# Optimization experiments

Hardware: AMD Instinct MI355X
Metric: run time of the kernel (lower is better)

## Reference

```python
import jax, jax.numpy as jnp
import numpy as np

B, S, D = 8, 4096, 256


def setup_inputs() -> dict:
    key = jax.random.key(0)
    kq, kk, kv, kb = jax.random.split(key, 4)
    q = jax.random.normal(kq, (B, S, D), dtype=jnp.float32)
    k = jax.random.normal(kk, (B, S, D), dtype=jnp.float32)
    v = jax.random.normal(kv, (B, S, D), dtype=jnp.float32)
    beta = jax.random.uniform(kb, (B, S), dtype=jnp.float32)
    return {"q": q, "k": k, "v": v, "beta": beta}


def reference(q, k, v, beta):
    # Delta-rule linear attention recurrence:
    #   h_t = beta_t * h_{t-1} + k_t^T v_t   (h: [B, D, D])
    #   o_t = q_t @ h_t                      (o: [B, D])
    dtype = q.dtype
    b, s, d = q.shape
    h0 = jnp.zeros((b, d, d), dtype=dtype)

    def step(h, inp):
        q_t, k_t, v_t, b_t = inp  # q_t/k_t/v_t: [B, D], b_t: [B]
        h = h * b_t[:, None, None] + jnp.einsum('bi,bj->bij', k_t, v_t)
        o_t = jnp.einsum('bi,bij->bj', q_t, h)
        return h, o_t

    xs = (q.transpose(1, 0, 2), k.transpose(1, 0, 2),
          v.transpose(1, 0, 2), beta.T)  # time-major
    _, out = jax.lax.scan(step, h0, xs)  # out: [S, B, D]
    return out.transpose(1, 0, 2)  # [B, S, D]
```

## Files before the change

### kernel.cpp

```cpp
#include <hip/hip_runtime.h>
#include <hip/hip_bf16.h>
#include <math.h>


#define B_ 8
#define S_ 4096
#define D_ 256
#define L_ 128
#define C_ (S_ / L_)
#define BC_ (B_ * C_)
#define STK 66

typedef __attribute__((ext_vector_type(8))) short s8v;
typedef __attribute__((ext_vector_type(4))) float f4v;
typedef unsigned short u16;
typedef unsigned int u32;

__device__ __forceinline__ u32 pk2(float lo, float hi) {
  union { __hip_bfloat162 h; u32 u; } cv;
  cv.h = __float22bfloat162_rn(make_float2(lo, hi));
  return cv.u;
}
__device__ __forceinline__ s8v pack8(const float4 a, const float4 b) {
  union { u32 u[4]; s8v v; } r;
  r.u[0] = pk2(a.x, a.y); r.u[1] = pk2(a.z, a.w);
  r.u[2] = pk2(b.x, b.y); r.u[3] = pk2(b.z, b.w);
  return r.v;
}

__device__ __forceinline__ void beta_scan128(const float* betap, float* ls,
                                             int tid) {
  if (tid < 64) {
    float x = log2f(fmaxf(betap[tid], 1e-30f));
#pragma unroll
    for (int off = 1; off < 64; off <<= 1) {
      float y = __shfl_up(x, off);
      if (tid >= off) x += y;
    }
    ls[tid] = x;
    const float tot0 = __shfl(x, 63);
    float z = log2f(fmaxf(betap[64 + tid], 1e-30f));
#pragma unroll
    for (int off = 1; off < 64; off <<= 1) {
      float y = __shfl_up(z, off);
      if (tid >= off) z += y;
    }
    ls[64 + tid] = z + tot0;
  }
}

__global__ __launch_bounds__(512, 2) void ks_summary6(
    const float* __restrict__ kg, const float* __restrict__ vg,
    const float* __restrict__ beta, u16* __restrict__ A,
    float* __restrict__ P)
{
  __shared__ float ls[L_];
  __shared__ __align__(16) u16 U[2][256 * STK];
  __shared__ __align__(16) u16 BN[64 * 264];

  const int bc = blockIdx.x;
  const int b = bc / C_, c = bc % C_;
  const int tid = threadIdx.x;
  const float* betap = beta + (size_t)b * S_ + (size_t)c * L_;
  const float* kbase = kg + ((size_t)b * S_ + (size_t)c * L_) * D_;
  const float* vbase = vg + ((size_t)b * S_ + (size_t)c * L_) * D_;

  beta_scan128(betap, ls, tid);
  __syncthreads();
  const float ltot = ls[L_ - 1];
  if (tid == 0) P[bc] = exp2f(ltot);

  const int hh = tid >> 8;
  const int t2 = tid & 255;
  const int iLs = t2 & 7;
  const int s0s = (t2 >> 3) * 2;
  const int sg = hh * 64 + s0s;

  {
    const float* src0 = kbase + (size_t)sg * D_;
    const float* src1 = src0 + D_;
    const float w0 = exp2f(ltot - ls[sg]);
    const float w1 = exp2f(ltot - ls[sg + 1]);
    u16* dst = U[hh];
#pragma unroll
    for (int p = 0; p < 8; ++p) {
      const int i0 = p * 32 + iLs * 4;
      float a0[4], a1[4];
      *(float4*)a0 = *(const float4*)(src0 + i0);
      *(float4*)a1 = *(const float4*)(src1 + i0);
#pragma unroll
      for (int u = 0; u < 4; ++u)
        *(u32*)&dst[(i0 + u) * STK + s0s] = pk2(a0[u] * w0, a1[u] * w1);
    }
  }
  __syncthreads();

  const int lane = tid & 63, wave = tid >> 6;
  const int quad = lane >> 4, l15 = lane & 15;
  const int i0w = wave * 32;

  s8v af[2][4];
#pragma unroll
  for (int mt = 0; mt < 2; ++mt)
#pragma unroll
    for (int ks = 0; ks < 4; ++ks)
      af[mt][ks] = *(const s8v*)&U[ks >> 1][(i0w + mt * 16 + l15) * STK +
                                            (ks & 1) * 32 + quad * 8];
  __syncthreads();

  {
    const float* src0 = vbase + (size_t)sg * D_;
    const float* src1 = src0 + D_;
    u16* dst = U[hh];
#pragma unroll
    for (int p = 0; p < 8; ++p) {
      const int i0 = p * 32 + iLs * 4;
      float a0[4], a1[4];
      *(float4*)a0 = *(const float4*)(src0 + i0);
      *(float4*)a1 = *(const float4*)(src1 + i0);
#pragma unroll
      for (int u = 0; u < 4; ++u)
        *(u32*)&dst[(i0 + u) * STK + s0s] = pk2(a0[u], a1[u]);
    }
  }
  __syncthreads();

  u16* Ab = A + (size_t)bc * D_ * D_;

  for (int ng = 0; ng < 4; ++ng) {
    f4v acc[2][4];
#pragma unroll
    for (int mt = 0; mt < 2; ++mt)
#pragma unroll
      for (int nt = 0; nt < 4; ++nt) acc[mt][nt] = (f4v){0.f, 0.f, 0.f, 0.f};

#pragma unroll
    for (int ks = 0; ks < 4; ++ks) {
      const int so = (ks & 1) * 32 + quad * 8;
      s8v bv[4];
#pragma unroll
      for (int nt = 0; nt < 4; ++nt)
        bv[nt] = *(const s8v*)&U[ks >> 1][(ng * 64 + nt * 16 + l15) * STK + so];
#pragma unroll
      for (int mt = 0; mt < 2; ++mt)
#pragma unroll
        for (int nt = 0; nt < 4; ++nt)
          acc[mt][nt] = __builtin_amdgcn_mfma_f32_16x16x32_bf16(
              af[mt][ks], bv[nt], acc[mt][nt], 0, 0, 0);
    }
#pragma unroll
    for (int mt = 0; mt < 2; ++mt)
#pragma unroll
      for (int nt = 0; nt < 4; ++nt) {
        const int jl = nt * 16 + l15;
        uint2 w;
        w.x = pk2(acc[mt][nt][0], acc[mt][nt][1]);
        w.y = pk2(acc[mt][nt][2], acc[mt][nt][3]);
        *(uint2*)&BN[jl * 264 + i0w + mt * 16 + quad * 4] = w;
      }
    __syncthreads();
    {
      const int jl = tid >> 3;
      const int il = (tid & 7) * 8;
#pragma unroll
      for (int p = 0; p < 4; ++p) {
        const int iu = il + p * 64;
        *(s8v*)&Ab[(size_t)(ng * 64 + jl) * D_ + iu] =
            *(const s8v*)&BN[jl * 264 + iu];
      }
    }
    __syncthreads();
  }
}

__global__ __launch_bounds__(256) void ks_scan6(
    u16* __restrict__ A, const float* __restrict__ P)
{
  const int g = blockIdx.x;
  const int b = g >> 6;
  const int unit = ((g & 63) << 8) + threadIdx.x;
  u16* base = A + (size_t)b * ((size_t)C_ * D_ * D_) + (size_t)unit * 4;
  const float* Pb = P + b * C_;

  uint2 d[C_];
#pragma unroll
  for (int c = 0; c < C_; ++c)
    d[c] = *(const uint2*)(base + (size_t)c * (D_ * D_));

  float h0 = 0.f, h1 = 0.f, h2 = 0.f, h3 = 0.f;
#pragma unroll
  for (int c = 0; c < C_; ++c) {
    const float pc = Pb[c];
    const uint2 u = d[c];
    const float a0 = __uint_as_float(u.x << 16);
    const float a1 = __uint_as_float(u.x & 0xFFFF0000u);
    const float a2 = __uint_as_float(u.y << 16);
    const float a3 = __uint_as_float(u.y & 0xFFFF0000u);
    d[c].x = pk2(h0, h1);
    d[c].y = pk2(h2, h3);
    h0 = fmaf(pc, h0, a0); h1 = fmaf(pc, h1, a1);
    h2 = fmaf(pc, h2, a2); h3 = fmaf(pc, h3, a3);
  }
#pragma unroll
  for (int c = 0; c < C_; ++c)
    *(uint2*)(base + (size_t)c * (D_ * D_)) = d[c];
}

__global__ __launch_bounds__(512, 2) void ks_output6(
    const float* __restrict__ qg, const float* __restrict__ kg,
    const float* __restrict__ vg, const float* __restrict__ beta,
    const u16* __restrict__ Hg, float* __restrict__ outg)
{
  __shared__ float ls[L_];
  __shared__ float cv[L_];
  __shared__ __align__(16) u16 QB[L_ * 264];
  __shared__ __align__(16) u16 Tm[L_ * 136];
  __shared__ __align__(16) u16 VT[256 * STK];

  const int bc = blockIdx.x;
  const int b = bc / C_, c = bc % C_;
  const int tid = threadIdx.x;
  const float* betap = beta + (size_t)b * S_ + (size_t)c * L_;
  const float* qbase = qg + ((size_t)b * S_ + (size_t)c * L_) * D_;
  const float* kbase = kg + ((size_t)b * S_ + (size_t)c * L_) * D_;
  const float* vbase = vg + ((size_t)b * S_ + (size_t)c * L_) * D_;
  const u16* Hb = Hg + (size_t)bc * D_ * D_;

  beta_scan128(betap, ls, tid);

  {
    const int t = tid >> 2;
    const int cg = (tid & 3) * 8;
    const float* src = qbase + (size_t)t * D_ + cg;
#pragma unroll
    for (int p = 0; p < 8; ++p) {
      const s8v pk = pack8(*(const float4*)(src + p * 32),
                           *(const float4*)(src + p * 32 + 4));
      *(s8v*)&QB[t * 264 + cg + p * 32] = pk;
    }
  }
  __syncthreads();
  if (tid < L_) cv[tid] = exp2f(ls[tid]);

  const int lane = tid & 63, wave = tid >> 6;
  const int quad = lane >> 4, l15 = lane & 15;
  const int j0w = wave * 32;

  {
    const int mA = wave * 16;
    f4v accA[8];
#pragma unroll
    for (int i = 0; i < 8; ++i) accA[i] = (f4v){0.f, 0.f, 0.f, 0.f};
#pragma unroll
    for (int kd = 0; kd < 8; ++kd) {
      const int d0 = kd * 32 + quad * 8;
      const float* krow = kbase + (size_t)(mA + l15) * D_ + d0;
      const s8v af = pack8(*(const float4*)krow, *(const float4*)(krow + 4));
#pragma unroll
      for (int nt = 0; nt < 8; ++nt) {
        const s8v bf = *(const s8v*)&QB[(nt * 16 + l15) * 264 + d0];
        accA[nt] = __builtin_amdgcn_mfma_f32_16x16x32_bf16(af, bf, accA[nt],
                                                           0, 0, 0);
      }
    }
#pragma unroll
    for (int nt = 0; nt < 8; ++nt) {
      const int t = nt * 16 + l15;
      const float lt = ls[t];
      const int s0 = mA + quad * 4;
      float v[4];
#pragma unroll
      for (int r = 0; r < 4; ++r) {
        const int s = s0 + r;
        v[r] = (s <= t) ? accA[nt][r] * exp2f(lt - ls[s]) : 0.f;
      }
      uint2 w;
      w.x = pk2(v[0], v[1]);
      w.y = pk2(v[2], v[3]);
      *(uint2*)&Tm[t * 136 + s0] = w;
    }
  }

  {
    const int iL = tid & 15;
    const int s0 = ((tid >> 4) & 31) * 2;
    const float* src0 = vbase + (size_t)s0 * D_;
    const float* src1 = src0 + D_;
#pragma unroll
    for (int p = 0; p < 4; ++p) {
      const int i0 = p * 64 + iL * 4;
      float a0[4], a1[4];
      *(float4*)a0 = *(const float4*)(src0 + i0);
      *(float4*)a1 = *(const float4*)(src1 + i0);
#pragma unroll
      for (int u = 0; u < 4; ++u)
        *(u32*)&VT[(i0 + u) * STK + s0] = pk2(a0[u], a1[u]);
    }
  }

  s8v hc[2];
#pragma unroll
  for (int mt = 0; mt < 2; ++mt)
    hc[mt] = *(const s8v*)(Hb + (size_t)(j0w + mt * 16 + l15) * D_ + quad * 8);

  __syncthreads();

  f4v acc[2][8];
#pragma unroll
  for (int mt = 0; mt < 2; ++mt)
#pragma unroll
    for (int nt = 0; nt < 8; ++nt) acc[mt][nt] = (f4v){0.f, 0.f, 0.f, 0.f};

#pragma unroll
  for (int ks = 0; ks < 8; ++ks) {
    const int io = ks * 32 + quad * 8;
    s8v hn[2] = {hc[0], hc[1]};
    if (ks < 7) {
#pragma unroll
      for (int mt = 0; mt < 2; ++mt)
        hn[mt] = *(const s8v*)(Hb + (size_t)(j0w + mt * 16 + l15) * D_ +
                               io + 32);
    }
    s8v bf[8];
#pragma unroll
    for (int nt = 0; nt < 8; ++nt)
      bf[nt] = *(const s8v*)&QB[(nt * 16 + l15) * 264 + io];
#pragma unroll
    for (int mt = 0; mt < 2; ++mt)
#pragma unroll
      for (int nt = 0; nt < 8; ++nt)
        acc[mt][nt] = __builtin_amdgcn_mfma_f32_16x16x32_bf16(
            hc[mt], bf[nt], acc[mt][nt], 0, 0, 0);
    hc[0] = hn[0]; hc[1] = hn[1];
  }
#pragma unroll
  for (int nt = 0; nt < 8; ++nt) {
    const float ct = cv[nt * 16 + l15];
#pragma unroll
    for (int mt = 0; mt < 2; ++mt) {
      acc[mt][nt][0] *= ct; acc[mt][nt][1] *= ct;
      acc[mt][nt][2] *= ct; acc[mt][nt][3] *= ct;
    }
  }

#pragma unroll
  for (int ks = 0; ks < 2; ++ks) {
    const int so = ks * 32 + quad * 8;
    s8v af[2], bf[8];
#pragma unroll
    for (int mt = 0; mt < 2; ++mt)
      af[mt] = *(const s8v*)&VT[(j0w + mt * 16 + l15) * STK + so];
#pragma unroll
    for (int nt = 0; nt < 8; ++nt)
      bf[nt] = *(const s8v*)&Tm[(nt * 16 + l15) * 136 + so];
#pragma unroll
    for (int mt = 0; mt < 2; ++mt)
#pragma unroll
      for (int nt = 0; nt < 8; ++nt)
        acc[mt][nt] = __builtin_amdgcn_mfma_f32_16x16x32_bf16(
            af[mt], bf[nt], acc[mt][nt], 0, 0, 0);
  }

  __syncthreads();
  {
    const int iL = tid & 15;
    const int s0 = ((tid >> 4) & 31) * 2;
    const float* src0 = vbase + (size_t)(64 + s0) * D_;
    const float* src1 = src0 + D_;
#pragma unroll
    for (int p = 0; p < 4; ++p) {
      const int i0 = p * 64 + iL * 4;
      float a0[4], a1[4];
      *(float4*)a0 = *(const float4*)(src0 + i0);
      *(float4*)a1 = *(const float4*)(src1 + i0);
#pragma unroll
      for (int u = 0; u < 4; ++u)
        *(u32*)&VT[(i0 + u) * STK + s0] = pk2(a0[u], a1[u]);
    }
  }
  __syncthreads();
#pragma unroll
  for (int ks = 0; ks < 2; ++ks) {
    const int so = ks * 32 + quad * 8;
    s8v af[2], bf[8];
#pragma unroll
    for (int mt = 0; mt < 2; ++mt)
      af[mt] = *(const s8v*)&VT[(j0w + mt * 16 + l15) * STK + so];
#pragma unroll
    for (int nt = 0; nt < 8; ++nt)
      bf[nt] = *(const s8v*)&Tm[(nt * 16 + l15) * 136 + 64 + so];
#pragma unroll
    for (int mt = 0; mt < 2; ++mt)
#pragma unroll
      for (int nt = 0; nt < 8; ++nt)
        acc[mt][nt] = __builtin_amdgcn_mfma_f32_16x16x32_bf16(
            af[mt], bf[nt], acc[mt][nt], 0, 0, 0);
  }

  float* ob = outg + ((size_t)b * S_ + (size_t)c * L_) * D_;
#pragma unroll
  for (int mt = 0; mt < 2; ++mt)
#pragma unroll
    for (int nt = 0; nt < 8; ++nt) {
      const int t = nt * 16 + l15;
      const int j0 = j0w + mt * 16 + quad * 4;
      float4 o;
      o.x = acc[mt][nt][0]; o.y = acc[mt][nt][1];
      o.z = acc[mt][nt][2]; o.w = acc[mt][nt][3];
      *(float4*)(ob + (size_t)t * D_ + j0) = o;
    }
}

extern "C" void kernel_launch(void* const* d_in, const int* in_sizes, int n_in,
                              void* d_out, int out_size, void* d_ws,
                              size_t ws_size, hipStream_t stream) {
  const float* q = (const float*)d_in[0];
  const float* k = (const float*)d_in[1];
  const float* v = (const float*)d_in[2];
  const float* beta = (const float*)d_in[3];
  float* out = (float*)d_out;

  u16* A = (u16*)d_ws;
  float* P = (float*)((char*)d_ws + (size_t)BC_ * D_ * D_ * sizeof(u16));

  ks_summary6<<<dim3(BC_), dim3(512), 0, stream>>>(k, v, beta, A, P);
  ks_scan6<<<dim3(512), dim3(256), 0, stream>>>(A, P);
  ks_output6<<<dim3(BC_), dim3(512), 0, stream>>>(q, k, v, beta, A, out);
}
```

Baseline: 172.0 us.

## Split summary and output kernels across two blocks per chunk for more parallelism

Both the chunk-summary and output kernels now launch two blocks per chunk: the summary kernel splits the output j columns in half, and the output kernel splits the 128 timesteps into two halves of 64. Shared memory per block is reduced (a single staging buffer, smaller QB/Tm/VT tiles with V staged in 32-row slices), and launch bounds are raised to allow 4 blocks per CU. With only 256 blocks before, the intent is to fill the GPU's CUs better and raise occupancy. In exchange, the K chunk (summary) and the beta scan plus intra-chunk K·Q work (output) are duplicated across the paired blocks, and the output kernel adds extra barriers.

Result: slower. 192.0 us (+11.6%).

```diff
diff --git a/kernel.cpp b/kernel.cpp
--- a/kernel.cpp
+++ b/kernel.cpp
@@ -9,7 +9,6 @@
 #define L_ 128
 #define C_ (S_ / L_)
 #define BC_ (B_ * C_)
-#define STK 66
 
 typedef __attribute__((ext_vector_type(8))) short s8v;
 typedef __attribute__((ext_vector_type(4))) float f4v;
@@ -49,16 +48,17 @@
   }
 }
 
-__global__ __launch_bounds__(512, 2) void ks_summary6(
+__global__ __launch_bounds__(512, 4) void ks_summary7(
     const float* __restrict__ kg, const float* __restrict__ vg,
     const float* __restrict__ beta, u16* __restrict__ A,
     float* __restrict__ P)
 {
   __shared__ float ls[L_];
-  __shared__ __align__(16) u16 U[2][256 * STK];
+  __shared__ __align__(16) u16 SB[256 * 66];
   __shared__ __align__(16) u16 BN[64 * 264];
 
-  const int bc = blockIdx.x;
+  const int bx = blockIdx.x;
+  const int bc = bx >> 1, jh = bx & 1;
   const int b = bc / C_, c = bc % C_;
   const int tid = threadIdx.x;
   const float* betap = beta + (size_t)b * S_ + (size_t)c * L_;
@@ -68,66 +68,71 @@
   beta_scan128(betap, ls, tid);
   __syncthreads();
   const float ltot = ls[L_ - 1];
-  if (tid == 0) P[bc] = exp2f(ltot);
-
-  const int hh = tid >> 8;
-  const int t2 = tid & 255;
-  const int iLs = t2 & 7;
-  const int s0s = (t2 >> 3) * 2;
-  const int sg = hh * 64 + s0s;
-
-  {
-    const float* src0 = kbase + (size_t)sg * D_;
-    const float* src1 = src0 + D_;
-    const float w0 = exp2f(ltot - ls[sg]);
-    const float w1 = exp2f(ltot - ls[sg + 1]);
-    u16* dst = U[hh];
-#pragma unroll
-    for (int p = 0; p < 8; ++p) {
-      const int i0 = p * 32 + iLs * 4;
-      float a0[4], a1[4];
-      *(float4*)a0 = *(const float4*)(src0 + i0);
-      *(float4*)a1 = *(const float4*)(src1 + i0);
-#pragma unroll
-      for (int u = 0; u < 4; ++u)
-        *(u32*)&dst[(i0 + u) * STK + s0s] = pk2(a0[u] * w0, a1[u] * w1);
-    }
-  }
-  __syncthreads();
+  if (tid == 0 && jh == 0) P[bc] = exp2f(ltot);
 
   const int lane = tid & 63, wave = tid >> 6;
   const int quad = lane >> 4, l15 = lane & 15;
   const int i0w = wave * 32;
 
   s8v af[2][4];
-#pragma unroll
-  for (int mt = 0; mt < 2; ++mt)
-#pragma unroll
-    for (int ks = 0; ks < 4; ++ks)
-      af[mt][ks] = *(const s8v*)&U[ks >> 1][(i0w + mt * 16 + l15) * STK +
-                                            (ks & 1) * 32 + quad * 8];
+
+#pragma unroll
+  for (int h = 0; h < 2; ++h) {
+    {
+      const int iL = tid & 15;
+      const int s0 = (tid >> 4) * 2;
+      const int sg = h * 64 + s0;
+      const float* src0 = kbase + (size_t)sg * D_;
+      const float* src1 = src0 + D_;
+      const float w0 = exp2f(ltot - ls[sg]);
+      const float w1 = exp2f(ltot - ls[sg + 1]);
+#pragma unroll
+      for (int p = 0; p < 4; ++p) {
+        const int i0 = p * 64 + iL * 4;
+        float a0[4], a1[4];
+        *(float4*)a0 = *(const float4*)(src0 + i0);
+        *(float4*)a1 = *(const float4*)(src1 + i0);
+#pragma unroll
+        for (int u = 0; u < 4; ++u)
+          *(u32*)&SB[(i0 + u) * 66 + s0] = pk2(a0[u] * w0, a1[u] * w1);
+      }
+    }
+    __syncthreads();
+#pragma unroll
+    for (int mt = 0; mt < 2; ++mt)
+#pragma unroll
+      for (int kk = 0; kk < 2; ++kk)
+        af[mt][h * 2 + kk] = *(const s8v*)&SB[(i0w + mt * 16 + l15) * 66 +
+                                              kk * 32 + quad * 8];
+    __syncthreads();
+  }
+
+  {
+    const int jL = tid & 15;
+    const int sp = tid >> 4;
+#pragma unroll
+    for (int h = 0; h < 2; ++h) {
+      const int s0 = sp * 2;
+      const int sg = h * 64 + s0;
+      const float* src0 = vbase + (size_t)sg * D_ + jh * 128;
+      const float* src1 = src0 + D_;
+#pragma unroll
+      for (int p = 0; p < 2; ++p) {
+        const int j0 = p * 64 + jL * 4;
+        float a0[4], a1[4];
+        *(float4*)a0 = *(const float4*)(src0 + j0);
+        *(float4*)a1 = *(const float4*)(src1 + j0);
+#pragma unroll
+        for (int u = 0; u < 4; ++u)
+          *(u32*)&SB[h * (128 * 66) + (j0 + u) * 66 + s0] = pk2(a0[u], a1[u]);
+      }
+    }
+  }
   __syncthreads();
 
-  {
-    const float* src0 = vbase + (size_t)sg * D_;
-    const float* src1 = src0 + D_;
-    u16* dst = U[hh];
-#pragma unroll
-    for (int p = 0; p < 8; ++p) {
-      const int i0 = p * 32 + iLs * 4;
-      float a0[4], a1[4];
-      *(float4*)a0 = *(const float4*)(src0 + i0);
-      *(float4*)a1 = *(const float4*)(src1 + i0);
-#pragma unroll
-      for (int u = 0; u < 4; ++u)
-        *(u32*)&dst[(i0 + u) * STK + s0s] = pk2(a0[u], a1[u]);
-    }
-  }
-  __syncthreads();
-
   u16* Ab = A + (size_t)bc * D_ * D_;
 
-  for (int ng = 0; ng < 4; ++ng) {
+  for (int ng = 0; ng < 2; ++ng) {
     f4v acc[2][4];
 #pragma unroll
     for (int mt = 0; mt < 2; ++mt)
@@ -140,7 +145,8 @@
       s8v bv[4];
 #pragma unroll
       for (int nt = 0; nt < 4; ++nt)
-        bv[nt] = *(const s8v*)&U[ks >> 1][(ng * 64 + nt * 16 + l15) * STK + so];
+        bv[nt] = *(const s8v*)&SB[(ks >> 1) * (128 * 66) +
+                                  (ng * 64 + nt * 16 + l15) * 66 + so];
 #pragma unroll
       for (int mt = 0; mt < 2; ++mt)
 #pragma unroll
@@ -162,18 +168,18 @@
     {
       const int jl = tid >> 3;
       const int il = (tid & 7) * 8;
+      const int jgl = jh * 128 + ng * 64 + jl;
 #pragma unroll
       for (int p = 0; p < 4; ++p) {
         const int iu = il + p * 64;
-        *(s8v*)&Ab[(size_t)(ng * 64 + jl) * D_ + iu] =
-            *(const s8v*)&BN[jl * 264 + iu];
-      }
-    }
-    __syncthreads();
-  }
-}
-
-__global__ __launch_bounds__(256) void ks_scan6(
+        *(s8v*)&Ab[(size_t)jgl * D_ + iu] = *(const s8v*)&BN[jl * 264 + iu];
+      }
+    }
+    __syncthreads();
+  }
+}
+
+__global__ __launch_bounds__(256) void ks_scan7(
     u16* __restrict__ A, const float* __restrict__ P)
 {
   const int g = blockIdx.x;
@@ -206,18 +212,19 @@
     *(uint2*)(base + (size_t)c * (D_ * D_)) = d[c];
 }
 
-__global__ __launch_bounds__(512, 2) void ks_output6(
+__global__ __launch_bounds__(512, 4) void ks_output7(
     const float* __restrict__ qg, const float* __restrict__ kg,
     const float* __restrict__ vg, const float* __restrict__ beta,
     const u16* __restrict__ Hg, float* __restrict__ outg)
 {
   __shared__ float ls[L_];
-  __shared__ float cv[L_];
-  __shared__ __align__(16) u16 QB[L_ * 264];
-  __shared__ __align__(16) u16 Tm[L_ * 136];
-  __shared__ __align__(16) u16 VT[256 * STK];
-
-  const int bc = blockIdx.x;
+  __shared__ float cv[64];
+  __shared__ __align__(16) u16 QB[64 * 264];
+  __shared__ __align__(16) u16 Tm[64 * 136];
+  __shared__ __align__(16) u16 VT[256 * 34];
+
+  const int bx = blockIdx.x;
+  const int bc = bx >> 1, th = bx & 1;
   const int b = bc / C_, c = bc % C_;
   const int tid = threadIdx.x;
   const float* betap = beta + (size_t)b * S_ + (size_t)c * L_;
@@ -229,87 +236,34 @@
   beta_scan128(betap, ls, tid);
 
   {
-    const int t = tid >> 2;
-    const int cg = (tid & 3) * 8;
-    const float* src = qbase + (size_t)t * D_ + cg;
-#pragma unroll
-    for (int p = 0; p < 8; ++p) {
-      const s8v pk = pack8(*(const float4*)(src + p * 32),
-                           *(const float4*)(src + p * 32 + 4));
-      *(s8v*)&QB[t * 264 + cg + p * 32] = pk;
+    const int t_loc = tid >> 3;
+    const int d8 = (tid & 7) * 8;
+    const float* src = qbase + (size_t)(th * 64 + t_loc) * D_;
+#pragma unroll
+    for (int p = 0; p < 4; ++p) {
+      const int d0 = d8 + p * 64;
+      const s8v pk = pack8(*(const float4*)(src + d0),
+                           *(const float4*)(src + d0 + 4));
+      *(s8v*)&QB[t_loc * 264 + d0] = pk;
     }
   }
   __syncthreads();
-  if (tid < L_) cv[tid] = exp2f(ls[tid]);
+  if (tid < 64) cv[tid] = exp2f(ls[th * 64 + tid]);
 
   const int lane = tid & 63, wave = tid >> 6;
   const int quad = lane >> 4, l15 = lane & 15;
   const int j0w = wave * 32;
 
-  {
-    const int mA = wave * 16;
-    f4v accA[8];
-#pragma unroll
-    for (int i = 0; i < 8; ++i) accA[i] = (f4v){0.f, 0.f, 0.f, 0.f};
-#pragma unroll
-    for (int kd = 0; kd < 8; ++kd) {
-      const int d0 = kd * 32 + quad * 8;
-      const float* krow = kbase + (size_t)(mA + l15) * D_ + d0;
-      const s8v af = pack8(*(const float4*)krow, *(const float4*)(krow + 4));
-#pragma unroll
-      for (int nt = 0; nt < 8; ++nt) {
-        const s8v bf = *(const s8v*)&QB[(nt * 16 + l15) * 264 + d0];
-        accA[nt] = __builtin_amdgcn_mfma_f32_16x16x32_bf16(af, bf, accA[nt],
-                                                           0, 0, 0);
-      }
-    }
-#pragma unroll
-    for (int nt = 0; nt < 8; ++nt) {
-      const int t = nt * 16 + l15;
-      const float lt = ls[t];
-      const int s0 = mA + quad * 4;
-      float v[4];
-#pragma unroll
-      for (int r = 0; r < 4; ++r) {
-        const int s = s0 + r;
-        v[r] = (s <= t) ? accA[nt][r] * exp2f(lt - ls[s]) : 0.f;
-      }
-      uint2 w;
-      w.x = pk2(v[0], v[1]);
-      w.y = pk2(v[2], v[3]);
-      *(uint2*)&Tm[t * 136 + s0] = w;
-    }
-  }
-
-  {
-    const int iL = tid & 15;
-    const int s0 = ((tid >> 4) & 31) * 2;
-    const float* src0 = vbase + (size_t)s0 * D_;
-    const float* src1 = src0 + D_;
-#pragma unroll
-    for (int p = 0; p < 4; ++p) {
-      const int i0 = p * 64 + iL * 4;
-      float a0[4], a1[4];
-      *(float4*)a0 = *(const float4*)(src0 + i0);
-      *(float4*)a1 = *(const float4*)(src1 + i0);
-#pragma unroll
-      for (int u = 0; u < 4; ++u)
-        *(u32*)&VT[(i0 + u) * STK + s0] = pk2(a0[u], a1[u]);
-    }
-  }
+  f4v acc[2][4];
+#pragma unroll
+  for (int mt = 0; mt < 2; ++mt)
+#pragma unroll
+    for (int nt = 0; nt < 4; ++nt) acc[mt][nt] = (f4v){0.f, 0.f, 0.f, 0.f};
 
   s8v hc[2];
 #pragma unroll
   for (int mt = 0; mt < 2; ++mt)
     hc[mt] = *(const s8v*)(Hb + (size_t)(j0w + mt * 16 + l15) * D_ + quad * 8);
-
-  __syncthreads();
-
-  f4v acc[2][8];
-#pragma unroll
-  for (int mt = 0; mt < 2; ++mt)
-#pragma unroll
-    for (int nt = 0; nt < 8; ++nt) acc[mt][nt] = (f4v){0.f, 0.f, 0.f, 0.f};
 
 #pragma unroll
   for (int ks = 0; ks < 8; ++ks) {
@@ -321,20 +275,20 @@
         hn[mt] = *(const s8v*)(Hb + (size_t)(j0w + mt * 16 + l15) * D_ +
                                io + 32);
     }
-    s8v bf[8];
-#pragma unroll
-    for (int nt = 0; nt < 8; ++nt)
+    s8v bf[4];
+#pragma unroll
+    for (int nt = 0; nt < 4; ++nt)
       bf[nt] = *(const s8v*)&QB[(nt * 16 + l15) * 264 + io];
 #pragma unroll
     for (int mt = 0; mt < 2; ++mt)
 #pragma unroll
-      for (int nt = 0; nt < 8; ++nt)
+      for (int nt = 0; nt < 4; ++nt)
         acc[mt][nt] = __builtin_amdgcn_mfma_f32_16x16x32_bf16(
             hc[mt], bf[nt], acc[mt][nt], 0, 0, 0);
     hc[0] = hn[0]; hc[1] = hn[1];
   }
 #pragma unroll
-  for (int nt = 0; nt < 8; ++nt) {
+  for (int nt = 0; nt < 4; ++nt) {
     const float ct = cv[nt * 16 + l15];
 #pragma unroll
     for (int mt = 0; mt < 2; ++mt) {
@@ -343,71 +297,92 @@
     }
   }
 
-#pragma unroll
-  for (int ks = 0; ks < 2; ++ks) {
-    const int so = ks * 32 + quad * 8;
-    s8v af[2], bf[8];
-#pragma unroll
-    for (int mt = 0; mt < 2; ++mt)
-      af[mt] = *(const s8v*)&VT[(j0w + mt * 16 + l15) * STK + so];
-#pragma unroll
-    for (int nt = 0; nt < 8; ++nt)
-      bf[nt] = *(const s8v*)&Tm[(nt * 16 + l15) * 136 + so];
-#pragma unroll
-    for (int mt = 0; mt < 2; ++mt)
-#pragma unroll
-      for (int nt = 0; nt < 8; ++nt)
+  {
+    const int mA = wave * 16;
+    f4v accA[4];
+#pragma unroll
+    for (int i = 0; i < 4; ++i) accA[i] = (f4v){0.f, 0.f, 0.f, 0.f};
+#pragma unroll
+    for (int kd = 0; kd < 8; ++kd) {
+      const int d0 = kd * 32 + quad * 8;
+      const float* krow = kbase + (size_t)(mA + l15) * D_ + d0;
+      const s8v afr = pack8(*(const float4*)krow, *(const float4*)(krow + 4));
+#pragma unroll
+      for (int nt = 0; nt < 4; ++nt) {
+        const s8v bf = *(const s8v*)&QB[(nt * 16 + l15) * 264 + d0];
+        accA[nt] = __builtin_amdgcn_mfma_f32_16x16x32_bf16(afr, bf, accA[nt],
+                                                           0, 0, 0);
+      }
+    }
+#pragma unroll
+    for (int nt = 0; nt < 4; ++nt) {
+      const int t_loc = nt * 16 + l15;
+      const int t = th * 64 + t_loc;
+      const float lt = ls[t];
+      const int s0 = mA + quad * 4;
+      float v[4];
+#pragma unroll
+      for (int r = 0; r < 4; ++r) {
+        const int s = s0 + r;
+        v[r] = (s <= t) ? accA[nt][r] * exp2f(lt - ls[s]) : 0.f;
+      }
+      uint2 w;
+      w.x = pk2(v[0], v[1]);
+      w.y = pk2(v[2], v[3]);
+      *(uint2*)&Tm[t_loc * 136 + s0] = w;
+    }
+  }
+
+#pragma unroll
+  for (int sq = 0; sq < 4; ++sq) {
+    __syncthreads();
+    {
+      const int jL = tid & 15;
+      const int sp = (tid >> 4) & 15;
+      const int hb = tid >> 8;
+      const int s0 = sp * 2;
+      const int sg = sq * 32 + s0;
+      const float* src0 = vbase + (size_t)sg * D_;
+      const float* src1 = src0 + D_;
+#pragma unroll
+      for (int p = 0; p < 2; ++p) {
+        const int j0 = hb * 128 + p * 64 + jL * 4;
+        float a0[4], a1[4];
+        *(float4*)a0 = *(const float4*)(src0 + j0);
+        *(float4*)a1 = *(const float4*)(src1 + j0);
+#pragma unroll
+        for (int u = 0; u < 4; ++u)
+          *(u32*)&VT[(j0 + u) * 34 + s0] = pk2(a0[u], a1[u]);
+      }
+    }
+    __syncthreads();
+    const int so = quad * 8;
+    s8v afv[2], bf[4];
+#pragma unroll
+    for (int mt = 0; mt < 2; ++mt)
+      afv[mt] = *(const s8v*)&VT[(j0w + mt * 16 + l15) * 34 + so];
+#pragma unroll
+    for (int nt = 0; nt < 4; ++nt)
+      bf[nt] = *(const s8v*)&Tm[(nt * 16 + l15) * 136 + sq * 32 + so];
+#pragma unroll
+    for (int mt = 0; mt < 2; ++mt)
+#pragma unroll
+      for (int nt = 0; nt < 4; ++nt)
         acc[mt][nt] = __builtin_amdgcn_mfma_f32_16x16x32_bf16(
-            af[mt], bf[nt], acc[mt][nt], 0, 0, 0);
-  }
-
-  __syncthreads();
-  {
-    const int iL = tid & 15;
-    const int s0 = ((tid >> 4) & 31) * 2;
-    const float* src0 = vbase + (size_t)(64 + s0) * D_;
-    const float* src1 = src0 + D_;
-#pragma unroll
-    for (int p = 0; p < 4; ++p) {
-      const int i0 = p * 64 + iL * 4;
-      float a0[4], a1[4];
-      *(float4*)a0 = *(const float4*)(src0 + i0);
-      *(float4*)a1 = *(const float4*)(src1 + i0);
-#pragma unroll
-      for (int u = 0; u < 4; ++u)
-        *(u32*)&VT[(i0 + u) * STK + s0] = pk2(a0[u], a1[u]);
-    }
-  }
-  __syncthreads();
-#pragma unroll
-  for (int ks = 0; ks < 2; ++ks) {
-    const int so = ks * 32 + quad * 8;
-    s8v af[2], bf[8];
-#pragma unroll
-    for (int mt = 0; mt < 2; ++mt)
-      af[mt] = *(const s8v*)&VT[(j0w + mt * 16 + l15) * STK + so];
-#pragma unroll
-    for (int nt = 0; nt < 8; ++nt)
-      bf[nt] = *(const s8v*)&Tm[(nt * 16 + l15) * 136 + 64 + so];
-#pragma unroll
-    for (int mt = 0; mt < 2; ++mt)
-#pragma unroll
-      for (int nt = 0; nt < 8; ++nt)
-        acc[mt][nt] = __builtin_amdgcn_mfma_f32_16x16x32_bf16(
-            af[mt], bf[nt], acc[mt][nt], 0, 0, 0);
-  }
-
-  float* ob = outg + ((size_t)b * S_ + (size_t)c * L_) * D_;
+            afv[mt], bf[nt], acc[mt][nt], 0, 0, 0);
+  }
+
+  float* ob = outg + ((size_t)b * S_ + (size_t)c * L_ + th * 64) * D_;
 #pragma unroll
   for (int mt = 0; mt < 2; ++mt)
 #pragma unroll
-    for (int nt = 0; nt < 8; ++nt) {
-      const int t = nt * 16 + l15;
+    for (int nt = 0; nt < 4; ++nt) {
+      const int t_loc = nt * 16 + l15;
       const int j0 = j0w + mt * 16 + quad * 4;
       float4 o;
       o.x = acc[mt][nt][0]; o.y = acc[mt][nt][1];
       o.z = acc[mt][nt][2]; o.w = acc[mt][nt][3];
-      *(float4*)(ob + (size_t)t * D_ + j0) = o;
+      *(float4*)(ob + (size_t)t_loc * D_ + j0) = o;
     }
 }
 
@@ -423,7 +398,7 @@
   u16* A = (u16*)d_ws;
   float* P = (float*)((char*)d_ws + (size_t)BC_ * D_ * D_ * sizeof(u16));
 
-  ks_summary6<<<dim3(BC_), dim3(512), 0, stream>>>(k, v, beta, A, P);
-  ks_scan6<<<dim3(512), dim3(256), 0, stream>>>(A, P);
-  ks_output6<<<dim3(BC_), dim3(512), 0, stream>>>(q, k, v, beta, A, out);
-}
+  ks_summary7<<<dim3(BC_ * 2), dim3(512), 0, stream>>>(k, v, beta, A, P);
+  ks_scan7<<<dim3(512), dim3(256), 0, stream>>>(A, P);
+  ks_output7<<<dim3(BC_ * 2), dim3(512), 0, stream>>>(q, k, v, beta, A, out);
+}
```

## Double threads per block to 1024 in summary and output kernels

Applied to the files above, without the earlier changes.

Moves the chunk-summary and chunk-output kernels from 512 to 1024 threads per block, halving each wave's MFMA tile (one 16-row tile instead of two) and re-partitioning the load/convert loops across the larger thread count. The aim is more waves in flight per chunk to hide global-load and LDS latency, with fewer registers per thread. In exchange, launch bounds drop to one block per CU, and each wave reloads shared B fragments for half the work, raising LDS traffic per MFMA.

After: 179.0 us. 4.1% more time.

```diff
diff --git a/kernel.cpp b/kernel.cpp
--- a/kernel.cpp
+++ b/kernel.cpp
@@ -9,7 +9,6 @@
 #define L_ 128
 #define C_ (S_ / L_)
 #define BC_ (B_ * C_)
-#define STK 66
 
 typedef __attribute__((ext_vector_type(8))) short s8v;
 typedef __attribute__((ext_vector_type(4))) float f4v;
@@ -49,13 +48,13 @@
   }
 }
 
-__global__ __launch_bounds__(512, 2) void ks_summary6(
+__global__ __launch_bounds__(1024, 1) void ks_summary8(
     const float* __restrict__ kg, const float* __restrict__ vg,
     const float* __restrict__ beta, u16* __restrict__ A,
     float* __restrict__ P)
 {
   __shared__ float ls[L_];
-  __shared__ __align__(16) u16 U[2][256 * STK];
+  __shared__ __align__(16) u16 U[2][256 * 66];
   __shared__ __align__(16) u16 BN[64 * 264];
 
   const int bc = blockIdx.x;
@@ -70,10 +69,11 @@
   const float ltot = ls[L_ - 1];
   if (tid == 0) P[bc] = exp2f(ltot);
 
-  const int hh = tid >> 8;
-  const int t2 = tid & 255;
-  const int iLs = t2 & 7;
-  const int s0s = (t2 >> 3) * 2;
+  const int hh = tid >> 9;
+  const int t2 = tid & 511;
+  const int iLs = t2 & 15;
+  const int sps = t2 >> 4;
+  const int s0s = sps * 2;
   const int sg = hh * 64 + s0s;
 
   {
@@ -83,29 +83,27 @@
     const float w1 = exp2f(ltot - ls[sg + 1]);
     u16* dst = U[hh];
 #pragma unroll
-    for (int p = 0; p < 8; ++p) {
-      const int i0 = p * 32 + iLs * 4;
+    for (int p = 0; p < 4; ++p) {
+      const int i0 = p * 64 + iLs * 4;
       float a0[4], a1[4];
       *(float4*)a0 = *(const float4*)(src0 + i0);
       *(float4*)a1 = *(const float4*)(src1 + i0);
 #pragma unroll
       for (int u = 0; u < 4; ++u)
-        *(u32*)&dst[(i0 + u) * STK + s0s] = pk2(a0[u] * w0, a1[u] * w1);
+        *(u32*)&dst[(i0 + u) * 66 + s0s] = pk2(a0[u] * w0, a1[u] * w1);
     }
   }
   __syncthreads();
 
   const int lane = tid & 63, wave = tid >> 6;
   const int quad = lane >> 4, l15 = lane & 15;
-  const int i0w = wave * 32;
-
-  s8v af[2][4];
-#pragma unroll
-  for (int mt = 0; mt < 2; ++mt)
-#pragma unroll
-    for (int ks = 0; ks < 4; ++ks)
-      af[mt][ks] = *(const s8v*)&U[ks >> 1][(i0w + mt * 16 + l15) * STK +
-                                            (ks & 1) * 32 + quad * 8];
+  const int i0w = wave * 16;
+
+  s8v af[4];
+#pragma unroll
+  for (int ks = 0; ks < 4; ++ks)
+    af[ks] = *(const s8v*)&U[ks >> 1][(i0w + l15) * 66 +
+                                      (ks & 1) * 32 + quad * 8];
   __syncthreads();
 
   {
@@ -113,14 +111,14 @@
     const float* src1 = src0 + D_;
     u16* dst = U[hh];
 #pragma unroll
-    for (int p = 0; p < 8; ++p) {
-      const int i0 = p * 32 + iLs * 4;
+    for (int p = 0; p < 4; ++p) {
+      const int i0 = p * 64 + iLs * 4;
       float a0[4], a1[4];
       *(float4*)a0 = *(const float4*)(src0 + i0);
       *(float4*)a1 = *(const float4*)(src1 + i0);
 #pragma unroll
       for (int u = 0; u < 4; ++u)
-        *(u32*)&dst[(i0 + u) * STK + s0s] = pk2(a0[u], a1[u]);
+        *(u32*)&dst[(i0 + u) * 66 + s0s] = pk2(a0[u], a1[u]);
     }
   }
   __syncthreads();
@@ -128,11 +126,9 @@
   u16* Ab = A + (size_t)bc * D_ * D_;
 
   for (int ng = 0; ng < 4; ++ng) {
-    f4v acc[2][4];
-#pragma unroll
-    for (int mt = 0; mt < 2; ++mt)
-#pragma unroll
-      for (int nt = 0; nt < 4; ++nt) acc[mt][nt] = (f4v){0.f, 0.f, 0.f, 0.f};
+    f4v acc[4];
+#pragma unroll
+    for (int nt = 0; nt < 4; ++nt) acc[nt] = (f4v){0.f, 0.f, 0.f, 0.f};
 
 #pragma unroll
     for (int ks = 0; ks < 4; ++ks) {
@@ -140,31 +136,27 @@
       s8v bv[4];
 #pragma unroll
       for (int nt = 0; nt < 4; ++nt)
-        bv[nt] = *(const s8v*)&U[ks >> 1][(ng * 64 + nt * 16 + l15) * STK + so];
-#pragma unroll
-      for (int mt = 0; mt < 2; ++mt)
-#pragma unroll
-        for (int nt = 0; nt < 4; ++nt)
-          acc[mt][nt] = __builtin_amdgcn_mfma_f32_16x16x32_bf16(
-              af[mt][ks], bv[nt], acc[mt][nt], 0, 0, 0);
-    }
-#pragma unroll
-    for (int mt = 0; mt < 2; ++mt)
-#pragma unroll
-      for (int nt = 0; nt < 4; ++nt) {
-        const int jl = nt * 16 + l15;
-        uint2 w;
-        w.x = pk2(acc[mt][nt][0], acc[mt][nt][1]);
-        w.y = pk2(acc[mt][nt][2], acc[mt][nt][3]);
-        *(uint2*)&BN[jl * 264 + i0w + mt * 16 + quad * 4] = w;
-      }
+        bv[nt] = *(const s8v*)&U[ks >> 1][(ng * 64 + nt * 16 + l15) * 66 + so];
+#pragma unroll
+      for (int nt = 0; nt < 4; ++nt)
+        acc[nt] = __builtin_amdgcn_mfma_f32_16x16x32_bf16(
+            af[ks], bv[nt], acc[nt], 0, 0, 0);
+    }
+#pragma unroll
+    for (int nt = 0; nt < 4; ++nt) {
+      const int jl = nt * 16 + l15;
+      uint2 w;
+      w.x = pk2(acc[nt][0], acc[nt][1]);
+      w.y = pk2(acc[nt][2], acc[nt][3]);
+      *(uint2*)&BN[jl * 264 + i0w + quad * 4] = w;
+    }
     __syncthreads();
     {
-      const int jl = tid >> 3;
-      const int il = (tid & 7) * 8;
-#pragma unroll
-      for (int p = 0; p < 4; ++p) {
-        const int iu = il + p * 64;
+      const int jl = tid >> 4;
+      const int il = (tid & 15) * 8;
+#pragma unroll
+      for (int p = 0; p < 2; ++p) {
+        const int iu = il + p * 128;
         *(s8v*)&Ab[(size_t)(ng * 64 + jl) * D_ + iu] =
             *(const s8v*)&BN[jl * 264 + iu];
       }
@@ -173,7 +165,7 @@
   }
 }
 
-__global__ __launch_bounds__(256) void ks_scan6(
+__global__ __launch_bounds__(256) void ks_scan8(
     u16* __restrict__ A, const float* __restrict__ P)
 {
   const int g = blockIdx.x;
@@ -206,7 +198,7 @@
     *(uint2*)(base + (size_t)c * (D_ * D_)) = d[c];
 }
 
-__global__ __launch_bounds__(512, 2) void ks_output6(
+__global__ __launch_bounds__(1024, 1) void ks_output8(
     const float* __restrict__ qg, const float* __restrict__ kg,
     const float* __restrict__ vg, const float* __restrict__ beta,
     const u16* __restrict__ Hg, float* __restrict__ outg)
@@ -215,7 +207,7 @@
   __shared__ float cv[L_];
   __shared__ __align__(16) u16 QB[L_ * 264];
   __shared__ __align__(16) u16 Tm[L_ * 136];
-  __shared__ __align__(16) u16 VT[256 * STK];
+  __shared__ __align__(16) u16 VT[256 * 66];
 
   const int bc = blockIdx.x;
   const int b = bc / C_, c = bc % C_;
@@ -229,14 +221,15 @@
   beta_scan128(betap, ls, tid);
 
   {
-    const int t = tid >> 2;
-    const int cg = (tid & 3) * 8;
-    const float* src = qbase + (size_t)t * D_ + cg;
-#pragma unroll
-    for (int p = 0; p < 8; ++p) {
-      const s8v pk = pack8(*(const float4*)(src + p * 32),
-                           *(const float4*)(src + p * 32 + 4));
-      *(s8v*)&QB[t * 264 + cg + p * 32] = pk;
+    const int t = tid >> 3;
+    const int d8 = (tid & 7) * 8;
+    const float* src = qbase + (size_t)t * D_;
+#pragma unroll
+    for (int p = 0; p < 4; ++p) {
+      const int d0 = d8 + p * 64;
+      const s8v pk = pack8(*(const float4*)(src + d0),
+                           *(const float4*)(src + d0 + 4));
+      *(s8v*)&QB[t * 264 + d0] = pk;
     }
   }
   __syncthreads();
@@ -244,28 +237,29 @@
 
   const int lane = tid & 63, wave = tid >> 6;
   const int quad = lane >> 4, l15 = lane & 15;
-  const int j0w = wave * 32;
-
-  {
-    const int mA = wave * 16;
-    f4v accA[8];
-#pragma unroll
-    for (int i = 0; i < 8; ++i) accA[i] = (f4v){0.f, 0.f, 0.f, 0.f};
+  const int j0w = wave * 16;
+
+  {
+    const int mA = (wave & 7) * 16;
+    const int tg = (wave >> 3) * 64;
+    f4v accA[4];
+#pragma unroll
+    for (int i = 0; i < 4; ++i) accA[i] = (f4v){0.f, 0.f, 0.f, 0.f};
 #pragma unroll
     for (int kd = 0; kd < 8; ++kd) {
       const int d0 = kd * 32 + quad * 8;
       const float* krow = kbase + (size_t)(mA + l15) * D_ + d0;
-      const s8v af = pack8(*(const float4*)krow, *(const float4*)(krow + 4));
-#pragma unroll
-      for (int nt = 0; nt < 8; ++nt) {
-        const s8v bf = *(const s8v*)&QB[(nt * 16 + l15) * 264 + d0];
-        accA[nt] = __builtin_amdgcn_mfma_f32_16x16x32_bf16(af, bf, accA[nt],
+      const s8v afr = pack8(*(const float4*)krow, *(const float4*)(krow + 4));
+#pragma unroll
+      for (int nt = 0; nt < 4; ++nt) {
+        const s8v bf = *(const s8v*)&QB[(tg + nt * 16 + l15) * 264 + d0];
+        accA[nt] = __builtin_amdgcn_mfma_f32_16x16x32_bf16(afr, bf, accA[nt],
                                                            0, 0, 0);
       }
     }
 #pragma unroll
-    for (int nt = 0; nt < 8; ++nt) {
-      const int t = nt * 16 + l15;
+    for (int nt = 0; nt < 4; ++nt) {
+      const int t = tg + nt * 16 + l15;
       const float lt = ls[t];
       const int s0 = mA + quad * 4;
       float v[4];
@@ -282,133 +276,113 @@
   }
 
   {
-    const int iL = tid & 15;
-    const int s0 = ((tid >> 4) & 31) * 2;
-    const float* src0 = vbase + (size_t)s0 * D_;
+    const int jL = tid & 15;
+    const int sp = (tid >> 4) & 31;
+    const int hb = tid >> 9;
+    const int s0 = sp * 2;
+    const float* src0 = vbase + (size_t)s0 * D_ + hb * 128;
     const float* src1 = src0 + D_;
 #pragma unroll
-    for (int p = 0; p < 4; ++p) {
-      const int i0 = p * 64 + iL * 4;
+    for (int p = 0; p < 2; ++p) {
+      const int j0 = hb * 128 + p * 64 + jL * 4;
       float a0[4], a1[4];
-      *(float4*)a0 = *(const float4*)(src0 + i0);
-      *(float4*)a1 = *(const float4*)(src1 + i0);
+      *(float4*)a0 = *(const float4*)(src0 + p * 64 + jL * 4);
+      *(float4*)a1 = *(const float4*)(src1 + p * 64 + jL * 4);
 #pragma unroll
       for (int u = 0; u < 4; ++u)
-        *(u32*)&VT[(i0 + u) * STK + s0] = pk2(a0[u], a1[u]);
-    }
-  }
-
-  s8v hc[2];
-#pragma unroll
-  for (int mt = 0; mt < 2; ++mt)
-    hc[mt] = *(const s8v*)(Hb + (size_t)(j0w + mt * 16 + l15) * D_ + quad * 8);
-
-  __syncthreads();
-
-  f4v acc[2][8];
-#pragma unroll
-  for (int mt = 0; mt < 2; ++mt)
-#pragma unroll
-    for (int nt = 0; nt < 8; ++nt) acc[mt][nt] = (f4v){0.f, 0.f, 0.f, 0.f};
+        *(u32*)&VT[(j0 + u) * 66 + s0] = pk2(a0[u], a1[u]);
+    }
+  }
+
+  s8v hc = *(const s8v*)(Hb + (size_t)(j0w + l15) * D_ + quad * 8);
+
+  __syncthreads();
+
+  f4v acc[8];
+#pragma unroll
+  for (int nt = 0; nt < 8; ++nt) acc[nt] = (f4v){0.f, 0.f, 0.f, 0.f};
 
 #pragma unroll
   for (int ks = 0; ks < 8; ++ks) {
     const int io = ks * 32 + quad * 8;
-    s8v hn[2] = {hc[0], hc[1]};
-    if (ks < 7) {
-#pragma unroll
-      for (int mt = 0; mt < 2; ++mt)
-        hn[mt] = *(const s8v*)(Hb + (size_t)(j0w + mt * 16 + l15) * D_ +
-                               io + 32);
-    }
+    s8v hn = hc;
+    if (ks < 7)
+      hn = *(const s8v*)(Hb + (size_t)(j0w + l15) * D_ + io + 32);
     s8v bf[8];
 #pragma unroll
     for (int nt = 0; nt < 8; ++nt)
       bf[nt] = *(const s8v*)&QB[(nt * 16 + l15) * 264 + io];
 #pragma unroll
-    for (int mt = 0; mt < 2; ++mt)
-#pragma unroll
-      for (int nt = 0; nt < 8; ++nt)
-        acc[mt][nt] = __builtin_amdgcn_mfma_f32_16x16x32_bf16(
-            hc[mt], bf[nt], acc[mt][nt], 0, 0, 0);
-    hc[0] = hn[0]; hc[1] = hn[1];
+    for (int nt = 0; nt < 8; ++nt)
+      acc[nt] = __builtin_amdgcn_mfma_f32_16x16x32_bf16(hc, bf[nt], acc[nt],
+                                                        0, 0, 0);
+    hc = hn;
   }
 #pragma unroll
   for (int nt = 0; nt < 8; ++nt) {
     const float ct = cv[nt * 16 + l15];
-#pragma unroll
-    for (int mt = 0; mt < 2; ++mt) {
-      acc[mt][nt][0] *= ct; acc[mt][nt][1] *= ct;
-      acc[mt][nt][2] *= ct; acc[mt][nt][3] *= ct;
-    }
+    acc[nt][0] *= ct; acc[nt][1] *= ct;
+    acc[nt][2] *= ct; acc[nt][3] *= ct;
   }
 
 #pragma unroll
   for (int ks = 0; ks < 2; ++ks) {
     const int so = ks * 32 + quad * 8;
-    s8v af[2], bf[8];
-#pragma unroll
-    for (int mt = 0; mt < 2; ++mt)
-      af[mt] = *(const s8v*)&VT[(j0w + mt * 16 + l15) * STK + so];
+    const s8v afv = *(const s8v*)&VT[(j0w + l15) * 66 + so];
+    s8v bf[8];
 #pragma unroll
     for (int nt = 0; nt < 8; ++nt)
       bf[nt] = *(const s8v*)&Tm[(nt * 16 + l15) * 136 + so];
 #pragma unroll
-    for (int mt = 0; mt < 2; ++mt)
-#pragma unroll
-      for (int nt = 0; nt < 8; ++nt)
-        acc[mt][nt] = __builtin_amdgcn_mfma_f32_16x16x32_bf16(
-            af[mt], bf[nt], acc[mt][nt], 0, 0, 0);
-  }
-
-  __syncthreads();
-  {
-    const int iL = tid & 15;
-    const int s0 = ((tid >> 4) & 31) * 2;
-    const float* src0 = vbase + (size_t)(64 + s0) * D_;
+    for (int nt = 0; nt < 8; ++nt)
+      acc[nt] = __builtin_amdgcn_mfma_f32_16x16x32_bf16(afv, bf[nt], acc[nt],
+                                                        0, 0, 0);
+  }
+
+  __syncthreads();
+  {
+    const int jL = tid & 15;
+    const int sp = (tid >> 4) & 31;
+    const int hb = tid >> 9;
+    const int s0 = sp * 2;
+    const float* src0 = vbase + (size_t)(64 + s0) * D_ + hb * 128;
     const float* src1 = src0 + D_;
 #pragma unroll
-    for (int p = 0; p < 4; ++p) {
-      const int i0 = p * 64 + iL * 4;
+    for (int p = 0; p < 2; ++p) {
+      const int j0 = hb * 128 + p * 64 + jL * 4;
       float a0[4], a1[4];
-      *(float4*)a0 = *(const float4*)(src0 + i0);
-      *(float4*)a1 = *(const float4*)(src1 + i0);
+      *(float4*)a0 = *(const float4*)(src0 + p * 64 + jL * 4);
+      *(float4*)a1 = *(const float4*)(src1 + p * 64 + jL * 4);
 #pragma unroll
       for (int u = 0; u < 4; ++u)
-        *(u32*)&VT[(i0 + u) * STK + s0] = pk2(a0[u], a1[u]);
+        *(u32*)&VT[(j0 + u) * 66 + s0] = pk2(a0[u], a1[u]);
     }
   }
   __syncthreads();
 #pragma unroll
   for (int ks = 0; ks < 2; ++ks) {
     const int so = ks * 32 + quad * 8;
-    s8v af[2], bf[8];
-#pragma unroll
-    for (int mt = 0; mt < 2; ++mt)
-      af[mt] = *(const s8v*)&VT[(j0w + mt * 16 + l15) * STK + so];
+    const s8v afv = *(const s8v*)&VT[(j0w + l15) * 66 + so];
+    s8v bf[8];
 #pragma unroll
     for (int nt = 0; nt < 8; ++nt)
       bf[nt] = *(const s8v*)&Tm[(nt * 16 + l15) * 136 + 64 + so];
 #pragma unroll
-    for (int mt = 0; mt < 2; ++mt)
-#pragma unroll
-      for (int nt = 0; nt < 8; ++nt)
-        acc[mt][nt] = __builtin_amdgcn_mfma_f32_16x16x32_bf16(
-            af[mt], bf[nt], acc[mt][nt], 0, 0, 0);
+    for (int nt = 0; nt < 8; ++nt)
+      acc[nt] = __builtin_amdgcn_mfma_f32_16x16x32_bf16(afv, bf[nt], acc[nt],
+                                                        0, 0, 0);
   }
 
   float* ob = outg + ((size_t)b * S_ + (size_t)c * L_) * D_;
 #pragma unroll
-  for (int mt = 0; mt < 2; ++mt)
-#pragma unroll
-    for (int nt = 0; nt < 8; ++nt) {
-      const int t = nt * 16 + l15;
-      const int j0 = j0w + mt * 16 + quad * 4;
-      float4 o;
-      o.x = acc[mt][nt][0]; o.y = acc[mt][nt][1];
-      o.z = acc[mt][nt][2]; o.w = acc[mt][nt][3];
-      *(float4*)(ob + (size_t)t * D_ + j0) = o;
-    }
+  for (int nt = 0; nt < 8; ++nt) {
+    const int t = nt * 16 + l15;
+    const int j0 = j0w + quad * 4;
+    float4 o;
+    o.x = acc[nt][0]; o.y = acc[nt][1];
+    o.z = acc[nt][2]; o.w = acc[nt][3];
+    *(float4*)(ob + (size_t)t * D_ + j0) = o;
+  }
 }
 
 extern "C" void kernel_launch(void* const* d_in, const int* in_sizes, int n_in,
@@ -423,7 +397,7 @@
   u16* A = (u16*)d_ws;
   float* P = (float*)((char*)d_ws + (size_t)BC_ * D_ * D_ * sizeof(u16));
 
-  ks_summary6<<<dim3(BC_), dim3(512), 0, stream>>>(k, v, beta, A, P);
-  ks_scan6<<<dim3(512), dim3(256), 0, stream>>>(A, P);
-  ks_output6<<<dim3(BC_), dim3(512), 0, stream>>>(q, k, v, beta, A, out);
-}
+  ks_summary8<<<dim3(BC_), dim3(1024), 0, stream>>>(k, v, beta, A, P);
+  ks_scan8<<<dim3(512), dim3(256), 0, stream>>>(A, P);
+  ks_output8<<<dim3(BC_), dim3(1024), 0, stream>>>(q, k, v, beta, A, out);
+}
```
